# Kernel tuning notes

Hardware: AMD Instinct MI355X
Metric: run time of the kernel (lower is better)

Reference implementation:

```python
import jax, jax.numpy as jnp
import numpy as np
import math

B, S, D, H = 2, 2048, 1024, 16
DK = D // H


def setup_inputs() -> dict:
    key = jax.random.key(0)
    ks = jax.random.split(key, 12)
    scale = 1.0 / math.sqrt(D)
    inp = {
        'query': jax.random.normal(ks[0], (B, S, D), dtype=jnp.float32),
        'key': jax.random.normal(ks[1], (B, S, D), dtype=jnp.float32),
        'value': jax.random.normal(ks[2], (B, S, D), dtype=jnp.float32),
        'mask': jnp.ones((B, 1, S), dtype=jnp.int32),
        'posr': jax.random.normal(ks[3], (B, S, S), dtype=jnp.float32),
        'Wq': jax.random.normal(ks[4], (D, D), dtype=jnp.float32) * scale,
        'bq': jnp.zeros((D,), dtype=jnp.float32),
        'Wk': jax.random.normal(ks[5], (D, D), dtype=jnp.float32) * scale,
        'bk': jnp.zeros((D,), dtype=jnp.float32),
        'Wv': jax.random.normal(ks[6], (D, D), dtype=jnp.float32) * scale,
        'bv': jnp.zeros((D,), dtype=jnp.float32),
        'Wo': jax.random.normal(ks[7], (D, D), dtype=jnp.float32) * scale,
        'bo': jnp.zeros((D,), dtype=jnp.float32),
    }
    return inp


def _split_heads(x):
    # [B, S, D] -> [B, H, S, DK]
    b, s, _ = x.shape
    return x.reshape(b, s, H, DK).transpose(0, 2, 1, 3)


def reference(query, key, value, mask, posr, Wq, bq, Wk, bk, Wv, bv, Wo, bo):
    q = _split_heads(query @ Wq.T + bq)   # [B,H,S,DK]
    k = _split_heads(key @ Wk.T + bk)
    v = _split_heads(value @ Wv.T + bv)

    scores = jnp.einsum('bhqd,bhkd->bhqk', q, k) / math.sqrt(DK)
    scores = scores + posr[:, None, :, :]            # additive positional bias
    m = mask[:, None, :, :]                           # [B,1,1,S] broadcast
    scores = jnp.where(m == 0, jnp.float32(-1e9), scores)
    p = jax.nn.softmax(scores, axis=-1)
    ctx = jnp.einsum('bhqk,bhkd->bhqd', p, v)        # [B,H,S,DK]
    ctx = ctx.transpose(0, 2, 1, 3).reshape(query.shape[0], -1, D)
    return ctx @ Wo.T + bo
```

## Files before the change

kernel.cpp:

```cpp
#include <hip/hip_runtime.h>
#include <math.h>

#define B_ 2
#define S_ 2048
#define D_ 1024
#define H_ 16
#define DK_ 64

typedef __attribute__((ext_vector_type(8))) short bf16x8;
typedef __attribute__((ext_vector_type(4))) float f32x4;

#define MFMA16(a, b, c) __builtin_amdgcn_mfma_f32_16x16x32_bf16((a), (b), (c), 0, 0, 0)

#define ASYNC16(g, l)                                                          \
    __builtin_amdgcn_global_load_lds(                                          \
        (const __attribute__((address_space(1))) void*)(g),                    \
        (__attribute__((address_space(3))) void*)(l), 16, 0, 0)

#define LOG2E 1.4426950408889634f

__device__ __forceinline__ unsigned short f2bf(float x) {
    unsigned int u = __float_as_uint(x);
    unsigned int r = (u + 0x7fffu + ((u >> 16) & 1u)) >> 16;
    return (unsigned short)r;
}

__global__ __launch_bounds__(256)
void pack_all(const float* __restrict__ q, const float* __restrict__ k,
              const float* __restrict__ v, const float* __restrict__ wq,
              const float* __restrict__ wk, const float* __restrict__ wv,
              const float* __restrict__ wo, unsigned short* __restrict__ ws0)
{
    const int z = blockIdx.z;
    const size_t IN = 4194304, WT = 1048576;
    const float* in;
    unsigned short* dst;
    int n;
    switch (z) {
        case 0: in = q;  dst = ws0;            n = (int)IN; break;
        case 1: in = k;  dst = ws0 + IN;       n = (int)IN; break;
        case 2: in = v;  dst = ws0 + 2*IN;     n = (int)IN; break;
        case 3: in = wq; dst = ws0 + 3*IN;          n = (int)WT; break;
        case 4: in = wk; dst = ws0 + 3*IN + WT;     n = (int)WT; break;
        case 5: in = wv; dst = ws0 + 3*IN + 2*WT;   n = (int)WT; break;
        default:in = wo; dst = ws0 + 3*IN + 3*WT;   n = (int)WT; break;
    }
    const int n4 = n >> 2;
    const int stride = gridDim.x * blockDim.x;
    for (int i = blockIdx.x * blockDim.x + threadIdx.x; i < n4; i += stride) {
        float4 x = ((const float4*)in)[i];
        ushort4 hv;
        hv.x = f2bf(x.x); hv.y = f2bf(x.y); hv.z = f2bf(x.z); hv.w = f2bf(x.w);
        ((ushort4*)dst)[i] = hv;
    }
}

__device__ __forceinline__ void gemm_core512(
    const unsigned short* __restrict__ A, const unsigned short* __restrict__ B,
    unsigned short* As, unsigned short* Bs, int m0, int n0, f32x4 (&acc)[4][2])
{
    const int tid  = threadIdx.x;
    const int w    = tid >> 6;
    const int lane = tid & 63;
    const int rA   = lane & 15;
    const int quad = lane >> 4;
    const int wm   = (w & 1) * 64;
    const int wn   = (w >> 1) * 32;

#pragma unroll 1
    for (int k0 = 0; k0 < 1024; k0 += 64) {
        __syncthreads();
#pragma unroll
        for (int i = 0; i < 2; ++i) {
            const int c   = i * 512 + tid;
            const int row = c >> 3;
            const int g   = (c & 7) ^ (row & 7);
            ASYNC16(A + (size_t)(m0 + row) * 1024 + k0 + g * 8,
                    As + (size_t)(i * 512 + w * 64) * 8);
            ASYNC16(B + (size_t)(n0 + row) * 1024 + k0 + g * 8,
                    Bs + (size_t)(i * 512 + w * 64) * 8);
        }
        __syncthreads();
#pragma unroll
        for (int ks = 0; ks < 2; ++ks) {
            bf16x8 a[4], bb2[2];
#pragma unroll
            for (int mt = 0; mt < 4; ++mt) {
                const int row = wm + mt * 16 + rA;
                a[mt] = *(const bf16x8*)&As[row * 64 + (((ks * 4 + quad) ^ (row & 7)) * 8)];
            }
#pragma unroll
            for (int nt = 0; nt < 2; ++nt) {
                const int row = wn + nt * 16 + rA;
                bb2[nt] = *(const bf16x8*)&Bs[row * 64 + (((ks * 4 + quad) ^ (row & 7)) * 8)];
            }
#pragma unroll
            for (int mt = 0; mt < 4; ++mt)
#pragma unroll
                for (int nt = 0; nt < 2; ++nt)
                    acc[mt][nt] = MFMA16(a[mt], bb2[nt], acc[mt][nt]);
        }
    }
}

__global__ __launch_bounds__(512, 4)
void gemm_qkv(const unsigned short* __restrict__ ws0,
              const float* __restrict__ bq, const float* __restrict__ bk,
              const float* __restrict__ bv,
              unsigned short* __restrict__ qbuf, unsigned short* __restrict__ kbuf,
              unsigned short* __restrict__ vtbuf)
{
    __shared__ unsigned short As[128 * 64];
    __shared__ unsigned short Bs[128 * 64];
    const size_t IN = 4194304, WT = 1048576;
    const int z = blockIdx.z;
    const unsigned short* Ap = ws0 + (size_t)z * IN;
    const unsigned short* Bp = ws0 + 3 * IN + (size_t)z * WT;
    const float* bias = (z == 0) ? bq : (z == 1) ? bk : bv;
    unsigned short* dst = (z == 0) ? qbuf : (z == 1) ? kbuf : vtbuf;

    const int m0 = blockIdx.y * 128;
    const int n0 = blockIdx.x * 128;
    f32x4 acc[4][2] = {};
    gemm_core512(Ap, Bp, As, Bs, m0, n0, acc);

    const int tid = threadIdx.x, w = tid >> 6, lane = tid & 63;
    const int quad = lane >> 4, col = lane & 15;
    const int wm = (w & 1) * 64, wn = (w >> 1) * 32;
    const float qscale = (z == 0) ? (0.125f * LOG2E) : 1.0f;
#pragma unroll
    for (int mt = 0; mt < 4; ++mt)
#pragma unroll
        for (int nt = 0; nt < 2; ++nt) {
            f32x4 v = acc[mt][nt];
#pragma unroll
            for (int r = 0; r < 4; ++r) {
                const int m = m0 + wm + mt * 16 + quad * 4 + r;
                const int n = n0 + wn + nt * 16 + col;
                const float val = (v[r] + bias[n]) * qscale;
                const int bb = m >> 11, ss = m & 2047;
                const int hh = n >> 6, dd = n & 63;
                if (z == 2)
                    dst[((size_t)(bb * 16 + hh) * 64 + dd) * 2048 + ss] = f2bf(val);
                else
                    dst[((size_t)(bb * 16 + hh) * 2048 + ss) * 64 + dd] = f2bf(val);
            }
        }
}

__global__ __launch_bounds__(512, 4)
void gemm_out(const unsigned short* __restrict__ Actx,
              const unsigned short* __restrict__ Bwo,
              const float* __restrict__ bias, float* __restrict__ out)
{
    __shared__ unsigned short As[128 * 64];
    __shared__ unsigned short Bs[128 * 64];
    const int m0 = blockIdx.y * 128;
    const int n0 = blockIdx.x * 128;
    f32x4 acc[4][2] = {};
    gemm_core512(Actx, Bwo, As, Bs, m0, n0, acc);

    const int tid = threadIdx.x, w = tid >> 6, lane = tid & 63;
    const int quad = lane >> 4, col = lane & 15;
    const int wm = (w & 1) * 64, wn = (w >> 1) * 32;
#pragma unroll
    for (int mt = 0; mt < 4; ++mt)
#pragma unroll
        for (int nt = 0; nt < 2; ++nt) {
            f32x4 v = acc[mt][nt];
#pragma unroll
            for (int r = 0; r < 4; ++r) {
                const int m = m0 + wm + mt * 16 + quad * 4 + r;
                const int n = n0 + wn + nt * 16 + col;
                out[(size_t)m * 1024 + n] = v[r] + bias[n];
            }
        }
}

__global__ __launch_bounds__(512, 4)
void attn_mfma(const unsigned short* __restrict__ qbuf,
               const unsigned short* __restrict__ kbuf,
               const unsigned short* __restrict__ vtbuf,
               const float* __restrict__ posr, const int* __restrict__ mask,
               unsigned short* __restrict__ ctxb)
{
    __shared__ unsigned short Ks[3][64 * 64];
    __shared__ unsigned short Vts[3][64 * 64];
    __shared__ unsigned short Ps[128 * 64];

    const int tid  = threadIdx.x;
    const int w    = tid >> 6;
    const int lane = tid & 63;
    const int quad = lane >> 4;
    const int col  = lane & 15;
    const int q0   = blockIdx.x * 128;
    const int h    = blockIdx.y;
    const int b    = blockIdx.z;
    const int wq   = w * 16;

    const size_t headoff = (size_t)(b * 16 + h) * 2048 * 64;
    const unsigned short* Qh  = qbuf + headoff + (size_t)q0 * 64;
    const unsigned short* Kh  = kbuf + headoff;
    const unsigned short* Vth = vtbuf + headoff;

    const int srow = tid >> 3;
    const int sg   = (tid & 7) ^ (srow & 7);

    bf16x8 qf[2];
#pragma unroll
    for (int ks = 0; ks < 2; ++ks)
        qf[ks] = *(const bf16x8*)&Qh[(size_t)(wq + col) * 64 + ks * 32 + quad * 8];

    ASYNC16(Kh + (size_t)srow * 64 + sg * 8,    &Ks[0][(size_t)(w * 64) * 8]);
    ASYNC16(Vth + (size_t)srow * 2048 + sg * 8, &Vts[0][(size_t)(w * 64) * 8]);

    f32x4 O[4] = {};
    float lsum[4] = {0.f, 0.f, 0.f, 0.f};

    const float* prq[4];
#pragma unroll
    for (int r = 0; r < 4; ++r)
        prq[r] = posr + ((size_t)b * 2048 + (q0 + wq + quad * 4 + r)) * 2048;
    const int* mrow = mask + (size_t)b * 2048;

    float pr[4][4];
#pragma unroll
    for (int r = 0; r < 4; ++r)
#pragma unroll
        for (int nt = 0; nt < 4; ++nt)
            pr[r][nt] = prq[r][nt * 16 + col];

    __syncthreads();

    f32x4 sc[4] = {};
#pragma unroll
    for (int ks = 0; ks < 2; ++ks)
#pragma unroll
        for (int nt = 0; nt < 4; ++nt) {
            const bf16x8 bk = *(const bf16x8*)
                &Ks[0][(nt * 16 + col) * 64 + (((ks * 4 + quad) ^ (col & 7)) * 8)];
            sc[nt] = MFMA16(qf[ks], bk, sc[nt]);
        }

    int bb = 0;
#pragma unroll 1
    for (int t = 0; t < 32; ++t) {
        const int k0 = t * 64;
        const int bn = (bb == 2) ? 0 : bb + 1;

        int mk[4];
#pragma unroll
        for (int nt = 0; nt < 4; ++nt) mk[nt] = mrow[k0 + nt * 16 + col];

        if (t < 31) {
            const int kn = k0 + 64;
            ASYNC16(Kh + (size_t)(kn + srow) * 64 + sg * 8,  &Ks[bn][(size_t)(w * 64) * 8]);
            ASYNC16(Vth + (size_t)srow * 2048 + kn + sg * 8, &Vts[bn][(size_t)(w * 64) * 8]);
        }

#pragma unroll
        for (int r = 0; r < 4; ++r) {
            const int rowW = wq + quad * 4 + r;
            const int rsw  = rowW & 7;
#pragma unroll
            for (int nt = 0; nt < 4; ++nt) {
                const float e = __builtin_amdgcn_exp2f(
                    fmaf(pr[r][nt], LOG2E, sc[nt][r]));
                unsigned int u = __float_as_uint(e) & 0xffff0000u;
                u = mk[nt] ? u : 0u;
                lsum[r] += __uint_as_float(u);
                const int kk = nt * 16 + col;
                Ps[rowW * 64 + ((((kk >> 3) ^ rsw)) * 8) + (kk & 7)] =
                    (unsigned short)(u >> 16);
            }
        }

        if (t < 31) __syncthreads();

#pragma unroll
        for (int ks = 0; ks < 2; ++ks) {
            const bf16x8 ap = *(const bf16x8*)
                &Ps[(wq + col) * 64 + (((ks * 4 + quad) ^ (col & 7)) * 8)];
#pragma unroll
            for (int nt = 0; nt < 4; ++nt) {
                const bf16x8 vb = *(const bf16x8*)
                    &Vts[bb][(nt * 16 + col) * 64 + (((ks * 4 + quad) ^ (col & 7)) * 8)];
                O[nt] = MFMA16(ap, vb, O[nt]);
            }
        }

        if (t < 31) {
            const int kn = k0 + 64;
#pragma unroll
            for (int r = 0; r < 4; ++r)
#pragma unroll
                for (int nt = 0; nt < 4; ++nt)
                    pr[r][nt] = prq[r][kn + nt * 16 + col];
#pragma unroll
            for (int nt = 0; nt < 4; ++nt) sc[nt] = (f32x4){0.f, 0.f, 0.f, 0.f};
#pragma unroll
            for (int ks = 0; ks < 2; ++ks)
#pragma unroll
                for (int nt = 0; nt < 4; ++nt) {
                    const bf16x8 bk = *(const bf16x8*)
                        &Ks[bn][(nt * 16 + col) * 64 + (((ks * 4 + quad) ^ (col & 7)) * 8)];
                    sc[nt] = MFMA16(qf[ks], bk, sc[nt]);
                }
        }
        bb = bn;
    }

#pragma unroll
    for (int r = 0; r < 4; ++r) {
#pragma unroll
        for (int o = 1; o < 16; o <<= 1) lsum[r] += __shfl_xor(lsum[r], o);
    }

#pragma unroll
    for (int r = 0; r < 4; ++r) {
        const float inv = 1.f / lsum[r];
        const size_t rowoff = ((size_t)b * 2048 + (q0 + wq + quad * 4 + r)) * 1024 + h * 64;
#pragma unroll
        for (int nt = 0; nt < 4; ++nt)
            ctxb[rowoff + nt * 16 + col] = f2bf(O[nt][r] * inv);
    }
}

extern "C" void kernel_launch(void* const* d_in, const int* in_sizes, int n_in,
                              void* d_out, int out_size, void* d_ws, size_t ws_size,
                              hipStream_t stream) {
    const float* query = (const float*)d_in[0];
    const float* key   = (const float*)d_in[1];
    const float* value = (const float*)d_in[2];
    const int*   mask  = (const int*)  d_in[3];
    const float* posr  = (const float*)d_in[4];
    const float* Wq    = (const float*)d_in[5];
    const float* bq    = (const float*)d_in[6];
    const float* Wk    = (const float*)d_in[7];
    const float* bk    = (const float*)d_in[8];
    const float* Wv    = (const float*)d_in[9];
    const float* bv    = (const float*)d_in[10];
    const float* Wo    = (const float*)d_in[11];
    const float* bo    = (const float*)d_in[12];
    float* out = (float*)d_out;

    unsigned short* ws0   = (unsigned short*)d_ws;
    const size_t IN = 4194304, WT = 1048576;
    unsigned short* qbuf  = ws0 + 4 * IN;
    unsigned short* kbuf  = ws0 + 5 * IN;
    unsigned short* vtbuf = ws0 + 6 * IN;
    unsigned short* ctxb  = ws0 + 7 * IN;
    const unsigned short* wob = ws0 + 3 * IN + 3 * WT;

    pack_all<<<dim3(512, 1, 7), 256, 0, stream>>>(query, key, value, Wq, Wk, Wv, Wo, ws0);

    gemm_qkv<<<dim3(8, 32, 3), 512, 0, stream>>>(ws0, bq, bk, bv, qbuf, kbuf, vtbuf);

    attn_mfma<<<dim3(16, 16, 2), 512, 0, stream>>>(qbuf, kbuf, vtbuf, posr, mask, ctxb);

    gemm_out<<<dim3(8, 32), 512, 0, stream>>>(ctxb, wob, bo, out);
}
```

Measured before the change: 272.3 us.

## Split attention keys and output columns across doubled waves with deeper K/V prefetch

The attention block grows from 512 to 1024 threads, so each query group of 16 rows is shared by two waves. Each wave computes scores and exp for half of the 64-key tile and accumulates half of the 64 output columns, and the per-row softmax sums are combined through shared memory at the end. K and V tile loads are split across the two thread halves and prefetched two tiles ahead, with a second barrier per iteration. The aim is more waves in flight to hide posr and K/V load latency. The cost is an extra barrier per step and tighter register limits from the new launch bounds, which could cause spills.

Result: slower. 488.8 us (+79.5%).

```diff
diff --git a/kernel.cpp b/kernel.cpp
--- a/kernel.cpp
+++ b/kernel.cpp
@@ -177,7 +177,7 @@
         }
 }
 
-__global__ __launch_bounds__(512, 4)
+__global__ __launch_bounds__(1024, 8)
 void attn_mfma(const unsigned short* __restrict__ qbuf,
                const unsigned short* __restrict__ kbuf,
                const unsigned short* __restrict__ vtbuf,
@@ -193,135 +193,158 @@
     const int lane = tid & 63;
     const int quad = lane >> 4;
     const int col  = lane & 15;
+    const int qg   = w >> 1;
+    const int kh   = w & 1;
     const int q0   = blockIdx.x * 128;
     const int h    = blockIdx.y;
     const int b    = blockIdx.z;
-    const int wq   = w * 16;
 
     const size_t headoff = (size_t)(b * 16 + h) * 2048 * 64;
     const unsigned short* Qh  = qbuf + headoff + (size_t)q0 * 64;
     const unsigned short* Kh  = kbuf + headoff;
     const unsigned short* Vth = vtbuf + headoff;
 
-    const int srow = tid >> 3;
-    const int sg   = (tid & 7) ^ (srow & 7);
+    const int sid  = tid & 511;
+    const int srow = sid >> 3;
+    const int sg   = (sid & 7) ^ (srow & 7);
+    const bool isK = (tid < 512);
 
     bf16x8 qf[2];
 #pragma unroll
     for (int ks = 0; ks < 2; ++ks)
-        qf[ks] = *(const bf16x8*)&Qh[(size_t)(wq + col) * 64 + ks * 32 + quad * 8];
-
-    ASYNC16(Kh + (size_t)srow * 64 + sg * 8,    &Ks[0][(size_t)(w * 64) * 8]);
-    ASYNC16(Vth + (size_t)srow * 2048 + sg * 8, &Vts[0][(size_t)(w * 64) * 8]);
-
-    f32x4 O[4] = {};
+        qf[ks] = *(const bf16x8*)&Qh[(size_t)(qg * 16 + col) * 64 + ks * 32 + quad * 8];
+
+    const float* prq[4];
+#pragma unroll
+    for (int r = 0; r < 4; ++r)
+        prq[r] = posr + ((size_t)b * 2048 + (q0 + qg * 16 + quad * 4 + r)) * 2048 + kh * 32;
+    const int* mrow = mask + (size_t)b * 2048 + kh * 32;
+
+    float pr[4][2];
+    int   mk[2];
+#pragma unroll
+    for (int r = 0; r < 4; ++r)
+#pragma unroll
+        for (int nt = 0; nt < 2; ++nt) pr[r][nt] = prq[r][nt * 16 + col];
+#pragma unroll
+    for (int nt = 0; nt < 2; ++nt) mk[nt] = mrow[nt * 16 + col];
+
+    if (isK) {
+        ASYNC16(Kh + (size_t)srow * 64 + sg * 8,         &Ks[0][(size_t)(w * 64) * 8]);
+        ASYNC16(Kh + (size_t)(64 + srow) * 64 + sg * 8,  &Ks[1][(size_t)(w * 64) * 8]);
+    } else {
+        ASYNC16(Vth + (size_t)srow * 2048 + sg * 8,      &Vts[0][(size_t)((w - 8) * 64) * 8]);
+        ASYNC16(Vth + (size_t)srow * 2048 + 64 + sg * 8, &Vts[1][(size_t)((w - 8) * 64) * 8]);
+    }
+
+    f32x4 O[2] = {};
+    f32x4 sc[2];
     float lsum[4] = {0.f, 0.f, 0.f, 0.f};
 
-    const float* prq[4];
-#pragma unroll
-    for (int r = 0; r < 4; ++r)
-        prq[r] = posr + ((size_t)b * 2048 + (q0 + wq + quad * 4 + r)) * 2048;
-    const int* mrow = mask + (size_t)b * 2048;
-
-    float pr[4][4];
-#pragma unroll
-    for (int r = 0; r < 4; ++r)
-#pragma unroll
-        for (int nt = 0; nt < 4; ++nt)
-            pr[r][nt] = prq[r][nt * 16 + col];
-
     __syncthreads();
 
-    f32x4 sc[4] = {};
+#pragma unroll
+    for (int nt = 0; nt < 2; ++nt) sc[nt] = (f32x4){0.f, 0.f, 0.f, 0.f};
 #pragma unroll
     for (int ks = 0; ks < 2; ++ks)
 #pragma unroll
-        for (int nt = 0; nt < 4; ++nt) {
+        for (int nt = 0; nt < 2; ++nt) {
             const bf16x8 bk = *(const bf16x8*)
-                &Ks[0][(nt * 16 + col) * 64 + (((ks * 4 + quad) ^ (col & 7)) * 8)];
+                &Ks[0][(kh * 32 + nt * 16 + col) * 64 + (((ks * 4 + quad) ^ (col & 7)) * 8)];
             sc[nt] = MFMA16(qf[ks], bk, sc[nt]);
         }
 
-    int bb = 0;
+    int bb = 0, b1 = 1, b2 = 2;
 #pragma unroll 1
     for (int t = 0; t < 32; ++t) {
-        const int k0 = t * 64;
-        const int bn = (bb == 2) ? 0 : bb + 1;
-
-        int mk[4];
-#pragma unroll
-        for (int nt = 0; nt < 4; ++nt) mk[nt] = mrow[k0 + nt * 16 + col];
-
-        if (t < 31) {
-            const int kn = k0 + 64;
-            ASYNC16(Kh + (size_t)(kn + srow) * 64 + sg * 8,  &Ks[bn][(size_t)(w * 64) * 8]);
-            ASYNC16(Vth + (size_t)srow * 2048 + kn + sg * 8, &Vts[bn][(size_t)(w * 64) * 8]);
-        }
-
 #pragma unroll
         for (int r = 0; r < 4; ++r) {
-            const int rowW = wq + quad * 4 + r;
+            const int rowW = qg * 16 + quad * 4 + r;
             const int rsw  = rowW & 7;
 #pragma unroll
-            for (int nt = 0; nt < 4; ++nt) {
+            for (int nt = 0; nt < 2; ++nt) {
                 const float e = __builtin_amdgcn_exp2f(
                     fmaf(pr[r][nt], LOG2E, sc[nt][r]));
                 unsigned int u = __float_as_uint(e) & 0xffff0000u;
                 u = mk[nt] ? u : 0u;
                 lsum[r] += __uint_as_float(u);
-                const int kk = nt * 16 + col;
-                Ps[rowW * 64 + ((((kk >> 3) ^ rsw)) * 8) + (kk & 7)] =
+                const int kk = kh * 32 + nt * 16 + col;
+                Ps[rowW * 64 + (((kk >> 3) ^ rsw) * 8) + (kk & 7)] =
                     (unsigned short)(u >> 16);
             }
         }
 
-        if (t < 31) __syncthreads();
+        __syncthreads();
+
+        if (t < 31) {
+            const int kn = (t + 1) * 64;
+#pragma unroll
+            for (int r = 0; r < 4; ++r)
+#pragma unroll
+                for (int nt = 0; nt < 2; ++nt) pr[r][nt] = prq[r][kn + nt * 16 + col];
+#pragma unroll
+            for (int nt = 0; nt < 2; ++nt) mk[nt] = mrow[kn + nt * 16 + col];
+        }
+        if (t < 30) {
+            const int kn = (t + 2) * 64;
+            if (isK) ASYNC16(Kh + (size_t)(kn + srow) * 64 + sg * 8,
+                             &Ks[b2][(size_t)(w * 64) * 8]);
+            else     ASYNC16(Vth + (size_t)srow * 2048 + kn + sg * 8,
+                             &Vts[b2][(size_t)((w - 8) * 64) * 8]);
+        }
 
 #pragma unroll
         for (int ks = 0; ks < 2; ++ks) {
             const bf16x8 ap = *(const bf16x8*)
-                &Ps[(wq + col) * 64 + (((ks * 4 + quad) ^ (col & 7)) * 8)];
-#pragma unroll
-            for (int nt = 0; nt < 4; ++nt) {
+                &Ps[(qg * 16 + col) * 64 + (((ks * 4 + quad) ^ (col & 7)) * 8)];
+#pragma unroll
+            for (int nt = 0; nt < 2; ++nt) {
                 const bf16x8 vb = *(const bf16x8*)
-                    &Vts[bb][(nt * 16 + col) * 64 + (((ks * 4 + quad) ^ (col & 7)) * 8)];
+                    &Vts[bb][(kh * 32 + nt * 16 + col) * 64 + (((ks * 4 + quad) ^ (col & 7)) * 8)];
                 O[nt] = MFMA16(ap, vb, O[nt]);
             }
         }
 
         if (t < 31) {
-            const int kn = k0 + 64;
-#pragma unroll
-            for (int r = 0; r < 4; ++r)
-#pragma unroll
-                for (int nt = 0; nt < 4; ++nt)
-                    pr[r][nt] = prq[r][kn + nt * 16 + col];
-#pragma unroll
-            for (int nt = 0; nt < 4; ++nt) sc[nt] = (f32x4){0.f, 0.f, 0.f, 0.f};
+#pragma unroll
+            for (int nt = 0; nt < 2; ++nt) sc[nt] = (f32x4){0.f, 0.f, 0.f, 0.f};
 #pragma unroll
             for (int ks = 0; ks < 2; ++ks)
 #pragma unroll
-                for (int nt = 0; nt < 4; ++nt) {
+                for (int nt = 0; nt < 2; ++nt) {
                     const bf16x8 bk = *(const bf16x8*)
-                        &Ks[bn][(nt * 16 + col) * 64 + (((ks * 4 + quad) ^ (col & 7)) * 8)];
+                        &Ks[b1][(kh * 32 + nt * 16 + col) * 64 + (((ks * 4 + quad) ^ (col & 7)) * 8)];
                     sc[nt] = MFMA16(qf[ks], bk, sc[nt]);
                 }
-        }
-        bb = bn;
-    }
+            asm volatile("s_waitcnt lgkmcnt(0)" ::: "memory");
+            __builtin_amdgcn_s_barrier();
+            asm volatile("" ::: "memory");
+        }
+        const int tmp = bb; bb = b1; b1 = b2; b2 = tmp;
+    }
+
+    __syncthreads();
 
 #pragma unroll
     for (int r = 0; r < 4; ++r) {
 #pragma unroll
         for (int o = 1; o < 16; o <<= 1) lsum[r] += __shfl_xor(lsum[r], o);
     }
+    float* Lred = (float*)&Ks[0][0];
+    if (col == 0) {
+#pragma unroll
+        for (int r = 0; r < 4; ++r)
+            Lred[kh * 128 + qg * 16 + quad * 4 + r] = lsum[r];
+    }
+    __syncthreads();
 
 #pragma unroll
     for (int r = 0; r < 4; ++r) {
-        const float inv = 1.f / lsum[r];
-        const size_t rowoff = ((size_t)b * 2048 + (q0 + wq + quad * 4 + r)) * 1024 + h * 64;
-#pragma unroll
-        for (int nt = 0; nt < 4; ++nt)
+        const int qloc = qg * 16 + quad * 4 + r;
+        const float inv = 1.f / (Lred[qloc] + Lred[128 + qloc]);
+        const size_t rowoff = ((size_t)b * 2048 + (q0 + qloc)) * 1024 + h * 64 + kh * 32;
+#pragma unroll
+        for (int nt = 0; nt < 2; ++nt)
             ctxb[rowoff + nt * 16 + col] = f2bf(O[nt][r] * inv);
     }
 }
@@ -356,7 +379,7 @@
 
     gemm_qkv<<<dim3(8, 32, 3), 512, 0, stream>>>(ws0, bq, bk, bv, qbuf, kbuf, vtbuf);
 
-    attn_mfma<<<dim3(16, 16, 2), 512, 0, stream>>>(qbuf, kbuf, vtbuf, posr, mask, ctxb);
+    attn_mfma<<<dim3(16, 16, 2), 1024, 0, stream>>>(qbuf, kbuf, vtbuf, posr, mask, ctxb);
 
     gemm_out<<<dim3(8, 32), 512, 0, stream>>>(ctxb, wob, bo, out);
 }
```

## Halve attention block to 4 waves with 32 query rows each and deeper K/V prefetch

Applied to the files above, without the earlier changes.

The attention kernel now runs 256 threads per block, each wave owning two 16-row query tiles. Each K/V fragment read from LDS feeds two MFMAs, which halves LDS traffic per MFMA. K/V staging is issued two tiles ahead instead of one, using a rotating triple buffer. The per-iteration barrier is replaced with an explicit waitcnt, s_barrier and sched_barrier sequence, and the mask loads are prefetched one tile ahead. In exchange, register pressure per wave roughly doubles and fewer waves per block are available to hide latency.

Result: no change. 273.1 us (+0.3%).

```diff
diff --git a/kernel.cpp b/kernel.cpp
--- a/kernel.cpp
+++ b/kernel.cpp
@@ -177,7 +177,7 @@
         }
 }
 
-__global__ __launch_bounds__(512, 4)
+__global__ __launch_bounds__(256, 2)
 void attn_mfma(const unsigned short* __restrict__ qbuf,
                const unsigned short* __restrict__ kbuf,
                const unsigned short* __restrict__ vtbuf,
@@ -196,134 +196,184 @@
     const int q0   = blockIdx.x * 128;
     const int h    = blockIdx.y;
     const int b    = blockIdx.z;
-    const int wq   = w * 16;
+    const int wq   = w * 32;
 
     const size_t headoff = (size_t)(b * 16 + h) * 2048 * 64;
     const unsigned short* Qh  = qbuf + headoff + (size_t)q0 * 64;
     const unsigned short* Kh  = kbuf + headoff;
     const unsigned short* Vth = vtbuf + headoff;
 
-    const int srow = tid >> 3;
-    const int sg   = (tid & 7) ^ (srow & 7);
-
-    bf16x8 qf[2];
-#pragma unroll
-    for (int ks = 0; ks < 2; ++ks)
-        qf[ks] = *(const bf16x8*)&Qh[(size_t)(wq + col) * 64 + ks * 32 + quad * 8];
-
-    ASYNC16(Kh + (size_t)srow * 64 + sg * 8,    &Ks[0][(size_t)(w * 64) * 8]);
-    ASYNC16(Vth + (size_t)srow * 2048 + sg * 8, &Vts[0][(size_t)(w * 64) * 8]);
-
-    f32x4 O[4] = {};
-    float lsum[4] = {0.f, 0.f, 0.f, 0.f};
-
-    const float* prq[4];
-#pragma unroll
-    for (int r = 0; r < 4; ++r)
-        prq[r] = posr + ((size_t)b * 2048 + (q0 + wq + quad * 4 + r)) * 2048;
+    const int c0 = tid;
+    const int c1 = 256 + tid;
+    const int r0 = c0 >> 3, g0 = (c0 & 7) ^ (r0 & 7);
+    const int r1 = c1 >> 3, g1 = (c1 & 7) ^ (r1 & 7);
+
+#define STAGE(bufidx, kt) do {                                                  \
+        ASYNC16(Kh + (size_t)((kt) * 64 + r0) * 64 + g0 * 8,                    \
+                &Ks[bufidx][(size_t)(w * 64) * 8]);                             \
+        ASYNC16(Kh + (size_t)((kt) * 64 + r1) * 64 + g1 * 8,                    \
+                &Ks[bufidx][(size_t)(256 + w * 64) * 8]);                       \
+        ASYNC16(Vth + (size_t)r0 * 2048 + (kt) * 64 + g0 * 8,                   \
+                &Vts[bufidx][(size_t)(w * 64) * 8]);                            \
+        ASYNC16(Vth + (size_t)r1 * 2048 + (kt) * 64 + g1 * 8,                   \
+                &Vts[bufidx][(size_t)(256 + w * 64) * 8]);                      \
+    } while (0)
+
+    bf16x8 qf[2][2];
+#pragma unroll
+    for (int mt = 0; mt < 2; ++mt)
+#pragma unroll
+        for (int ks = 0; ks < 2; ++ks)
+            qf[mt][ks] = *(const bf16x8*)
+                &Qh[(size_t)(wq + mt * 16 + col) * 64 + ks * 32 + quad * 8];
+
+    const float* prq[2][4];
+#pragma unroll
+    for (int mt = 0; mt < 2; ++mt)
+#pragma unroll
+        for (int r = 0; r < 4; ++r)
+            prq[mt][r] = posr +
+                ((size_t)b * 2048 + (q0 + wq + mt * 16 + quad * 4 + r)) * 2048;
     const int* mrow = mask + (size_t)b * 2048;
 
-    float pr[4][4];
-#pragma unroll
-    for (int r = 0; r < 4; ++r)
-#pragma unroll
-        for (int nt = 0; nt < 4; ++nt)
-            pr[r][nt] = prq[r][nt * 16 + col];
+    STAGE(0, 0);
+    STAGE(1, 1);
+
+    float pr[2][4][4];
+    int   mk[4];
+#pragma unroll
+    for (int mt = 0; mt < 2; ++mt)
+#pragma unroll
+        for (int r = 0; r < 4; ++r)
+#pragma unroll
+            for (int nt = 0; nt < 4; ++nt)
+                pr[mt][r][nt] = prq[mt][r][nt * 16 + col];
+#pragma unroll
+    for (int nt = 0; nt < 4; ++nt) mk[nt] = mrow[nt * 16 + col];
+
+    f32x4 sc[2][4];
+    f32x4 O[2][4] = {};
+    float lsum[2][4] = {{0.f, 0.f, 0.f, 0.f}, {0.f, 0.f, 0.f, 0.f}};
 
     __syncthreads();
 
-    f32x4 sc[4] = {};
-#pragma unroll
-    for (int ks = 0; ks < 2; ++ks)
-#pragma unroll
-        for (int nt = 0; nt < 4; ++nt) {
+#pragma unroll
+    for (int mt = 0; mt < 2; ++mt)
+#pragma unroll
+        for (int nt = 0; nt < 4; ++nt) sc[mt][nt] = (f32x4){0.f, 0.f, 0.f, 0.f};
+#pragma unroll
+    for (int nt = 0; nt < 4; ++nt)
+#pragma unroll
+        for (int ks = 0; ks < 2; ++ks) {
             const bf16x8 bk = *(const bf16x8*)
                 &Ks[0][(nt * 16 + col) * 64 + (((ks * 4 + quad) ^ (col & 7)) * 8)];
-            sc[nt] = MFMA16(qf[ks], bk, sc[nt]);
-        }
-
-    int bb = 0;
+#pragma unroll
+            for (int mt = 0; mt < 2; ++mt)
+                sc[mt][nt] = MFMA16(qf[mt][ks], bk, sc[mt][nt]);
+        }
+
+    int bb = 0, b1 = 1, b2 = 2;
 #pragma unroll 1
     for (int t = 0; t < 32; ++t) {
-        const int k0 = t * 64;
-        const int bn = (bb == 2) ? 0 : bb + 1;
-
-        int mk[4];
-#pragma unroll
-        for (int nt = 0; nt < 4; ++nt) mk[nt] = mrow[k0 + nt * 16 + col];
+#pragma unroll
+        for (int mt = 0; mt < 2; ++mt)
+#pragma unroll
+            for (int r = 0; r < 4; ++r) {
+                const int rowW = wq + mt * 16 + quad * 4 + r;
+                const int rsw  = rowW & 7;
+#pragma unroll
+                for (int nt = 0; nt < 4; ++nt) {
+                    const float e = __builtin_amdgcn_exp2f(
+                        fmaf(pr[mt][r][nt], LOG2E, sc[mt][nt][r]));
+                    unsigned int u = __float_as_uint(e) & 0xffff0000u;
+                    u = mk[nt] ? u : 0u;
+                    lsum[mt][r] += __uint_as_float(u);
+                    const int kk = nt * 16 + col;
+                    Ps[rowW * 64 + (((kk >> 3) ^ rsw) * 8) + (kk & 7)] =
+                        (unsigned short)(u >> 16);
+                }
+            }
+
+        __builtin_amdgcn_sched_barrier(0);
+        asm volatile("s_waitcnt lgkmcnt(0)" ::: "memory");
+        __builtin_amdgcn_s_barrier();
+        __builtin_amdgcn_sched_barrier(0);
+
+        if (t < 30) STAGE(b2, t + 2);
+        __builtin_amdgcn_sched_barrier(0);
 
         if (t < 31) {
-            const int kn = k0 + 64;
-            ASYNC16(Kh + (size_t)(kn + srow) * 64 + sg * 8,  &Ks[bn][(size_t)(w * 64) * 8]);
-            ASYNC16(Vth + (size_t)srow * 2048 + kn + sg * 8, &Vts[bn][(size_t)(w * 64) * 8]);
-        }
-
-#pragma unroll
-        for (int r = 0; r < 4; ++r) {
-            const int rowW = wq + quad * 4 + r;
-            const int rsw  = rowW & 7;
-#pragma unroll
-            for (int nt = 0; nt < 4; ++nt) {
-                const float e = __builtin_amdgcn_exp2f(
-                    fmaf(pr[r][nt], LOG2E, sc[nt][r]));
-                unsigned int u = __float_as_uint(e) & 0xffff0000u;
-                u = mk[nt] ? u : 0u;
-                lsum[r] += __uint_as_float(u);
-                const int kk = nt * 16 + col;
-                Ps[rowW * 64 + ((((kk >> 3) ^ rsw)) * 8) + (kk & 7)] =
-                    (unsigned short)(u >> 16);
-            }
-        }
-
-        if (t < 31) __syncthreads();
+            const int kn = (t + 1) * 64;
+#pragma unroll
+            for (int mt = 0; mt < 2; ++mt)
+#pragma unroll
+                for (int r = 0; r < 4; ++r)
+#pragma unroll
+                    for (int nt = 0; nt < 4; ++nt)
+                        pr[mt][r][nt] = prq[mt][r][kn + nt * 16 + col];
+#pragma unroll
+            for (int nt = 0; nt < 4; ++nt) mk[nt] = mrow[kn + nt * 16 + col];
+        }
 
 #pragma unroll
         for (int ks = 0; ks < 2; ++ks) {
-            const bf16x8 ap = *(const bf16x8*)
-                &Ps[(wq + col) * 64 + (((ks * 4 + quad) ^ (col & 7)) * 8)];
+            bf16x8 pa[2];
+#pragma unroll
+            for (int mt = 0; mt < 2; ++mt)
+                pa[mt] = *(const bf16x8*)
+                    &Ps[(wq + mt * 16 + col) * 64 + (((ks * 4 + quad) ^ (col & 7)) * 8)];
 #pragma unroll
             for (int nt = 0; nt < 4; ++nt) {
                 const bf16x8 vb = *(const bf16x8*)
                     &Vts[bb][(nt * 16 + col) * 64 + (((ks * 4 + quad) ^ (col & 7)) * 8)];
-                O[nt] = MFMA16(ap, vb, O[nt]);
+#pragma unroll
+                for (int mt = 0; mt < 2; ++mt)
+                    O[mt][nt] = MFMA16(pa[mt], vb, O[mt][nt]);
             }
         }
 
         if (t < 31) {
-            const int kn = k0 + 64;
-#pragma unroll
-            for (int r = 0; r < 4; ++r)
+#pragma unroll
+            for (int mt = 0; mt < 2; ++mt)
 #pragma unroll
                 for (int nt = 0; nt < 4; ++nt)
-                    pr[r][nt] = prq[r][kn + nt * 16 + col];
-#pragma unroll
-            for (int nt = 0; nt < 4; ++nt) sc[nt] = (f32x4){0.f, 0.f, 0.f, 0.f};
-#pragma unroll
-            for (int ks = 0; ks < 2; ++ks)
-#pragma unroll
-                for (int nt = 0; nt < 4; ++nt) {
+                    sc[mt][nt] = (f32x4){0.f, 0.f, 0.f, 0.f};
+#pragma unroll
+            for (int nt = 0; nt < 4; ++nt)
+#pragma unroll
+                for (int ks = 0; ks < 2; ++ks) {
                     const bf16x8 bk = *(const bf16x8*)
-                        &Ks[bn][(nt * 16 + col) * 64 + (((ks * 4 + quad) ^ (col & 7)) * 8)];
-                    sc[nt] = MFMA16(qf[ks], bk, sc[nt]);
+                        &Ks[b1][(nt * 16 + col) * 64 + (((ks * 4 + quad) ^ (col & 7)) * 8)];
+#pragma unroll
+                    for (int mt = 0; mt < 2; ++mt)
+                        sc[mt][nt] = MFMA16(qf[mt][ks], bk, sc[mt][nt]);
                 }
         }
-        bb = bn;
+        const int tmp = bb; bb = b1; b1 = b2; b2 = tmp;
     }
 
 #pragma unroll
-    for (int r = 0; r < 4; ++r) {
-#pragma unroll
-        for (int o = 1; o < 16; o <<= 1) lsum[r] += __shfl_xor(lsum[r], o);
-    }
-
-#pragma unroll
-    for (int r = 0; r < 4; ++r) {
-        const float inv = 1.f / lsum[r];
-        const size_t rowoff = ((size_t)b * 2048 + (q0 + wq + quad * 4 + r)) * 1024 + h * 64;
-#pragma unroll
-        for (int nt = 0; nt < 4; ++nt)
-            ctxb[rowoff + nt * 16 + col] = f2bf(O[nt][r] * inv);
-    }
+    for (int mt = 0; mt < 2; ++mt)
+#pragma unroll
+        for (int r = 0; r < 4; ++r) {
+#pragma unroll
+            for (int o = 1; o < 16; o <<= 1)
+                lsum[mt][r] += __shfl_xor(lsum[mt][r], o);
+        }
+
+#pragma unroll
+    for (int mt = 0; mt < 2; ++mt)
+#pragma unroll
+        for (int r = 0; r < 4; ++r) {
+            const float inv = 1.f / lsum[mt][r];
+            const int rowW = wq + mt * 16 + quad * 4 + r;
+            const size_t rowoff =
+                ((size_t)b * 2048 + (q0 + rowW)) * 1024 + h * 64;
+#pragma unroll
+            for (int nt = 0; nt < 4; ++nt)
+                ctxb[rowoff + nt * 16 + col] = f2bf(O[mt][nt][r] * inv);
+        }
+#undef STAGE
 }
 
 extern "C" void kernel_launch(void* const* d_in, const int* in_sizes, int n_in,
@@ -356,7 +406,7 @@
 
     gemm_qkv<<<dim3(8, 32, 3), 512, 0, stream>>>(ws0, bq, bk, bv, qbuf, kbuf, vtbuf);
 
-    attn_mfma<<<dim3(16, 16, 2), 512, 0, stream>>>(qbuf, kbuf, vtbuf, posr, mask, ctxb);
+    attn_mfma<<<dim3(16, 16, 2), 256, 0, stream>>>(qbuf, kbuf, vtbuf, posr, mask, ctxb);
 
     gemm_out<<<dim3(8, 32), 512, 0, stream>>>(ctxb, wob, bo, out);
 }
```

## Warp-specialize attention into QK/softmax and PV producer-consumer wavegroups

Applied to the files above, without the earlier changes.

The attention kernel is split into two wave groups. Waves 0-3 compute QK scores, add the positional bias, apply exp and write P tiles. Waves 4-7 load V tiles and run the PV MFMAs one step behind, using double-buffered P/K/V in LDS. The row sum is now an MFMA against a ones vector rather than a scalar accumulation, and masking is folded into the exponent input. Each wave now handles 32 query rows instead of 16, which raises register use and leaves half the waves idle for MFMA or exp work at any moment.

After: 545.0 us. 2x slower.

```diff
diff --git a/kernel.cpp b/kernel.cpp
--- a/kernel.cpp
+++ b/kernel.cpp
@@ -184,9 +184,9 @@
                const float* __restrict__ posr, const int* __restrict__ mask,
                unsigned short* __restrict__ ctxb)
 {
-    __shared__ unsigned short Ks[3][64 * 64];
-    __shared__ unsigned short Vts[3][64 * 64];
-    __shared__ unsigned short Ps[128 * 64];
+    __shared__ unsigned short Ks[2][64 * 64];
+    __shared__ unsigned short Vts[2][64 * 64];
+    __shared__ unsigned short Ps[2][128 * 64];
 
     const int tid  = threadIdx.x;
     const int w    = tid >> 6;
@@ -196,133 +196,154 @@
     const int q0   = blockIdx.x * 128;
     const int h    = blockIdx.y;
     const int b    = blockIdx.z;
-    const int wq   = w * 16;
+    const int wg   = w & 3;
+    const int wq   = wg * 32;
+    const bool isQK = (w < 4);
 
     const size_t headoff = (size_t)(b * 16 + h) * 2048 * 64;
     const unsigned short* Qh  = qbuf + headoff + (size_t)q0 * 64;
     const unsigned short* Kh  = kbuf + headoff;
     const unsigned short* Vth = vtbuf + headoff;
 
-    const int srow = tid >> 3;
-    const int sg   = (tid & 7) ^ (srow & 7);
-
-    bf16x8 qf[2];
-#pragma unroll
-    for (int ks = 0; ks < 2; ++ks)
-        qf[ks] = *(const bf16x8*)&Qh[(size_t)(wq + col) * 64 + ks * 32 + quad * 8];
-
-    ASYNC16(Kh + (size_t)srow * 64 + sg * 8,    &Ks[0][(size_t)(w * 64) * 8]);
-    ASYNC16(Vth + (size_t)srow * 2048 + sg * 8, &Vts[0][(size_t)(w * 64) * 8]);
-
-    f32x4 O[4] = {};
-    float lsum[4] = {0.f, 0.f, 0.f, 0.f};
-
-    const float* prq[4];
-#pragma unroll
-    for (int r = 0; r < 4; ++r)
-        prq[r] = posr + ((size_t)b * 2048 + (q0 + wq + quad * 4 + r)) * 2048;
+    const int st = tid & 255;
+    const int r0 = st >> 3;
+    const int g0 = (st & 7) ^ (r0 & 7);
+    const int r1 = r0 + 32;
+
+    bf16x8 qf[2][2];
+    if (isQK) {
+#pragma unroll
+        for (int mt = 0; mt < 2; ++mt)
+#pragma unroll
+            for (int ks = 0; ks < 2; ++ks)
+                qf[mt][ks] = *(const bf16x8*)
+                    &Qh[(size_t)(wq + mt * 16 + col) * 64 + ks * 32 + quad * 8];
+    }
+
+    const float* prb = posr + ((size_t)b * 2048 + (q0 + wq + quad * 4)) * 2048;
     const int* mrow = mask + (size_t)b * 2048;
 
-    float pr[4][4];
-#pragma unroll
-    for (int r = 0; r < 4; ++r)
-#pragma unroll
-        for (int nt = 0; nt < 4; ++nt)
-            pr[r][nt] = prq[r][nt * 16 + col];
-
+    const short one = (short)0x3F80;
+    const bf16x8 ones = {one, one, one, one, one, one, one, one};
+
+    f32x4 O[2][4] = {};
+    f32x4 lacc[2] = {};
+
+    if (isQK) {
+        ASYNC16(Kh + (size_t)r0 * 64 + g0 * 8, &Ks[0][(size_t)(wg * 64) * 8]);
+        ASYNC16(Kh + (size_t)r1 * 64 + g0 * 8, &Ks[0][(size_t)(256 + wg * 64) * 8]);
+    }
     __syncthreads();
 
-    f32x4 sc[4] = {};
-#pragma unroll
-    for (int ks = 0; ks < 2; ++ks)
-#pragma unroll
-        for (int nt = 0; nt < 4; ++nt) {
-            const bf16x8 bk = *(const bf16x8*)
-                &Ks[0][(nt * 16 + col) * 64 + (((ks * 4 + quad) ^ (col & 7)) * 8)];
-            sc[nt] = MFMA16(qf[ks], bk, sc[nt]);
-        }
-
-    int bb = 0;
 #pragma unroll 1
-    for (int t = 0; t < 32; ++t) {
-        const int k0 = t * 64;
-        const int bn = (bb == 2) ? 0 : bb + 1;
-
-        int mk[4];
-#pragma unroll
-        for (int nt = 0; nt < 4; ++nt) mk[nt] = mrow[k0 + nt * 16 + col];
-
-        if (t < 31) {
-            const int kn = k0 + 64;
-            ASYNC16(Kh + (size_t)(kn + srow) * 64 + sg * 8,  &Ks[bn][(size_t)(w * 64) * 8]);
-            ASYNC16(Vth + (size_t)srow * 2048 + kn + sg * 8, &Vts[bn][(size_t)(w * 64) * 8]);
-        }
-
-#pragma unroll
-        for (int r = 0; r < 4; ++r) {
-            const int rowW = wq + quad * 4 + r;
-            const int rsw  = rowW & 7;
-#pragma unroll
-            for (int nt = 0; nt < 4; ++nt) {
-                const float e = __builtin_amdgcn_exp2f(
-                    fmaf(pr[r][nt], LOG2E, sc[nt][r]));
-                unsigned int u = __float_as_uint(e) & 0xffff0000u;
-                u = mk[nt] ? u : 0u;
-                lsum[r] += __uint_as_float(u);
-                const int kk = nt * 16 + col;
-                Ps[rowW * 64 + ((((kk >> 3) ^ rsw)) * 8) + (kk & 7)] =
-                    (unsigned short)(u >> 16);
-            }
-        }
-
-        if (t < 31) __syncthreads();
-
-#pragma unroll
-        for (int ks = 0; ks < 2; ++ks) {
-            const bf16x8 ap = *(const bf16x8*)
-                &Ps[(wq + col) * 64 + (((ks * 4 + quad) ^ (col & 7)) * 8)];
-#pragma unroll
-            for (int nt = 0; nt < 4; ++nt) {
-                const bf16x8 vb = *(const bf16x8*)
-                    &Vts[bb][(nt * 16 + col) * 64 + (((ks * 4 + quad) ^ (col & 7)) * 8)];
-                O[nt] = MFMA16(ap, vb, O[nt]);
-            }
-        }
-
-        if (t < 31) {
-            const int kn = k0 + 64;
-#pragma unroll
-            for (int r = 0; r < 4; ++r)
+    for (int i = 0; i <= 32; ++i) {
+        const int cur = i & 1;
+        const int nxt = cur ^ 1;
+
+        if (isQK) {
+            if (i < 32) {
+                const int k0 = i * 64;
+                if (i < 31) {
+                    ASYNC16(Kh + (size_t)(k0 + 64 + r0) * 64 + g0 * 8,
+                            &Ks[nxt][(size_t)(wg * 64) * 8]);
+                    ASYNC16(Kh + (size_t)(k0 + 64 + r1) * 64 + g0 * 8,
+                            &Ks[nxt][(size_t)(256 + wg * 64) * 8]);
+                }
+                int mkv[4];
+#pragma unroll
+                for (int nt = 0; nt < 4; ++nt) mkv[nt] = mrow[k0 + nt * 16 + col];
+
+                f32x4 sc[2][4];
+#pragma unroll
+                for (int mt = 0; mt < 2; ++mt)
+#pragma unroll
+                    for (int nt = 0; nt < 4; ++nt)
+                        sc[mt][nt] = (f32x4){0.f, 0.f, 0.f, 0.f};
 #pragma unroll
                 for (int nt = 0; nt < 4; ++nt)
-                    pr[r][nt] = prq[r][kn + nt * 16 + col];
-#pragma unroll
-            for (int nt = 0; nt < 4; ++nt) sc[nt] = (f32x4){0.f, 0.f, 0.f, 0.f};
-#pragma unroll
-            for (int ks = 0; ks < 2; ++ks)
-#pragma unroll
-                for (int nt = 0; nt < 4; ++nt) {
-                    const bf16x8 bk = *(const bf16x8*)
-                        &Ks[bn][(nt * 16 + col) * 64 + (((ks * 4 + quad) ^ (col & 7)) * 8)];
-                    sc[nt] = MFMA16(qf[ks], bk, sc[nt]);
+#pragma unroll
+                    for (int ks = 0; ks < 2; ++ks) {
+                        const bf16x8 bk = *(const bf16x8*)
+                            &Ks[cur][(nt * 16 + col) * 64 +
+                                     (((ks * 4 + quad) ^ (col & 7)) * 8)];
+#pragma unroll
+                        for (int mt = 0; mt < 2; ++mt)
+                            sc[mt][nt] = MFMA16(qf[mt][ks], bk, sc[mt][nt]);
+                    }
+
+#pragma unroll
+                for (int mt = 0; mt < 2; ++mt) {
+                    float prv[4][4];
+#pragma unroll
+                    for (int r = 0; r < 4; ++r)
+#pragma unroll
+                        for (int nt = 0; nt < 4; ++nt)
+                            prv[r][nt] = prb[(size_t)(mt * 16 + r) * 2048 +
+                                             k0 + nt * 16 + col];
+#pragma unroll
+                    for (int r = 0; r < 4; ++r) {
+                        const int rowW = wq + mt * 16 + quad * 4 + r;
+                        const int rsw  = rowW & 7;
+#pragma unroll
+                        for (int nt = 0; nt < 4; ++nt) {
+                            const float pe = mkv[nt] ? prv[r][nt] : -1.0e30f;
+                            const float e = __builtin_amdgcn_exp2f(
+                                fmaf(pe, LOG2E, sc[mt][nt][r]));
+                            const int kk = nt * 16 + col;
+                            Ps[cur][rowW * 64 + (((kk >> 3) ^ rsw) * 8) + (kk & 7)] =
+                                (unsigned short)(__float_as_uint(e) >> 16);
+                        }
+                    }
                 }
-        }
-        bb = bn;
-    }
-
-#pragma unroll
-    for (int r = 0; r < 4; ++r) {
-#pragma unroll
-        for (int o = 1; o < 16; o <<= 1) lsum[r] += __shfl_xor(lsum[r], o);
-    }
-
-#pragma unroll
-    for (int r = 0; r < 4; ++r) {
-        const float inv = 1.f / lsum[r];
-        const size_t rowoff = ((size_t)b * 2048 + (q0 + wq + quad * 4 + r)) * 1024 + h * 64;
-#pragma unroll
-        for (int nt = 0; nt < 4; ++nt)
-            ctxb[rowoff + nt * 16 + col] = f2bf(O[nt][r] * inv);
+            }
+        } else {
+            if (i < 32) {
+                const int k0 = i * 64;
+                ASYNC16(Vth + (size_t)r0 * 2048 + k0 + g0 * 8,
+                        &Vts[cur][(size_t)(wg * 64) * 8]);
+                ASYNC16(Vth + (size_t)r1 * 2048 + k0 + g0 * 8,
+                        &Vts[cur][(size_t)(256 + wg * 64) * 8]);
+            }
+            if (i > 0) {
+#pragma unroll
+                for (int ks = 0; ks < 2; ++ks) {
+                    bf16x8 pa[2];
+#pragma unroll
+                    for (int mt = 0; mt < 2; ++mt)
+                        pa[mt] = *(const bf16x8*)
+                            &Ps[nxt][(wq + mt * 16 + col) * 64 +
+                                     (((ks * 4 + quad) ^ (col & 7)) * 8)];
+#pragma unroll
+                    for (int nt = 0; nt < 4; ++nt) {
+                        const bf16x8 vb = *(const bf16x8*)
+                            &Vts[nxt][(nt * 16 + col) * 64 +
+                                      (((ks * 4 + quad) ^ (col & 7)) * 8)];
+#pragma unroll
+                        for (int mt = 0; mt < 2; ++mt)
+                            O[mt][nt] = MFMA16(pa[mt], vb, O[mt][nt]);
+                    }
+#pragma unroll
+                    for (int mt = 0; mt < 2; ++mt)
+                        lacc[mt] = MFMA16(pa[mt], ones, lacc[mt]);
+                }
+            }
+        }
+        __syncthreads();
+    }
+
+    if (!isQK) {
+#pragma unroll
+        for (int mt = 0; mt < 2; ++mt)
+#pragma unroll
+            for (int r = 0; r < 4; ++r) {
+                const float inv = 1.f / lacc[mt][r];
+                const int rowW = wq + mt * 16 + quad * 4 + r;
+                const size_t rowoff =
+                    ((size_t)b * 2048 + (q0 + rowW)) * 1024 + h * 64;
+#pragma unroll
+                for (int nt = 0; nt < 4; ++nt)
+                    ctxb[rowoff + nt * 16 + col] = f2bf(O[mt][nt][r] * inv);
+            }
     }
 }
 
```
